# Performance work log

Measured on AMD Instinct MI355X. Metric: run time of the kernel, lower is better.

The kernel has to match this reference:

```python
import jax, jax.numpy as jnp
import numpy as np

H = 16  # GRU hidden size

def gru_dir(x, Wih, Whh, bih, bhh, reverse=False):
    # x: [B, T, D]; torch gate order: r, z, n
    def step(h, xt):
        gx = xt @ Wih.T + bih          # [B, 3H]
        gh = h @ Whh.T + bhh
        xr, xz, xn = jnp.split(gx, 3, axis=-1)
        hr, hz, hn = jnp.split(gh, 3, axis=-1)
        r = jax.nn.sigmoid(xr + hr)
        z = jax.nn.sigmoid(xz + hz)
        n = jnp.tanh(xn + r * hn)
        h_new = (1.0 - z) * n + z * h
        return h_new, h_new
    xs = jnp.swapaxes(x, 0, 1)         # [T, B, D]
    h0 = jnp.zeros((x.shape[0], H), x.dtype)
    _, hs = jax.lax.scan(step, h0, xs, reverse=reverse)
    return jnp.swapaxes(hs, 0, 1)      # [B, T, H]

def gru_bidir(x, pf, pb):
    f = gru_dir(x, *pf, reverse=False)
    b = gru_dir(x, *pb, reverse=True)
    return jnp.concatenate([f, b], axis=-1)   # [B, T, 2H]

def attention(h, Wa, ba, ctx):
    # h: [B, T, 2H]
    a = jnp.tanh(h @ Wa.T + ba)                # [B, T, 2H]
    w = jax.nn.softmax(a @ ctx, axis=1)        # [B, T]
    return jnp.einsum('bt,btd->bd', w, h), w

def setup_inputs() -> dict:
    key = jax.random.key(0)
    ks = iter(jax.random.split(key, 32))
    B, N, T, D, M = 64, 128, 128, 25, 16
    def p(shape, scale=0.1):
        return jax.random.normal(next(ks), shape, jnp.float32) * scale
    inp = {'x': jax.random.normal(next(ks), (B, N, T, D), jnp.float32)}
    # first bidirectional GRU (input 25)
    for sfx, din in [('1f', D), ('1b', D), ('2f', M), ('2b', M)]:
        inp['Wih' + sfx] = p((3 * H, din))
        inp['Whh' + sfx] = p((3 * H, H))
        inp['bih' + sfx] = p((3 * H,))
        inp['bhh' + sfx] = p((3 * H,))
    for sfx in ['1', '2']:
        inp['Wa' + sfx] = p((2 * H, 2 * H))
        inp['ba' + sfx] = p((2 * H,))
        inp['ctx' + sfx] = p((2 * H,))
    inp['Wm'] = p((M, 2 * H))
    inp['bm'] = p((M,))
    return inp

def reference(x, Wih1f, Whh1f, bih1f, bhh1f, Wih1b, Whh1b, bih1b, bhh1b,
              Wa1, ba1, ctx1, Wm, bm,
              Wih2f, Whh2f, bih2f, bhh2f, Wih2b, Whh2b, bih2b, bhh2b,
              Wa2, ba2, ctx2):
    B, N, T, D = x.shape
    xs = x.reshape(B * N, T, D)
    h1 = gru_bidir(xs, (Wih1f, Whh1f, bih1f, bhh1f), (Wih1b, Whh1b, bih1b, bhh1b))
    cv1, _ = attention(h1, Wa1, ba1, ctx1)          # [B*N, 2H]
    flow = (cv1 @ Wm.T + bm).reshape(B, N, -1)      # [B, N, M]
    h2 = gru_bidir(flow, (Wih2f, Whh2f, bih2f, bhh2f), (Wih2b, Whh2b, bih2b, bhh2b))
    cv2, _ = attention(h2, Wa2, ba2, ctx2)          # [B, 2H]
    return cv2
```

## Files before the change

### kernel.cpp

```cpp
#include <hip/hip_runtime.h>
#include <hip/hip_bf16.h>
#include <math.h>

#define TSTEPS 128
#define HD 16
#define AD 32
#define CHUNK 8
#define NCHK 16
#define H1W 36
#define SEQ_HALFS 4096
#define PH 264

#define SC1 1.44269504088896340736f
#define SC2 2.88539008177792681472f

typedef _Float16 h4 __attribute__((ext_vector_type(4)));
typedef _Float16 f16x8 __attribute__((ext_vector_type(8)));
typedef float f32x4 __attribute__((ext_vector_type(4)));

#if defined(__has_builtin)
#  if __has_builtin(__builtin_amdgcn_exp2f)
#    define EXP2F(x) __builtin_amdgcn_exp2f(x)
#  endif
#  if __has_builtin(__builtin_amdgcn_rcpf)
#    define RCPF(x) __builtin_amdgcn_rcpf(x)
#  endif
#  if __has_builtin(__builtin_amdgcn_global_load_lds)
#    define HAS_GLDS 1
#  endif
#endif
#ifndef EXP2F
#  define EXP2F(x) exp2f(x)
#endif
#ifndef RCPF
#  define RCPF(x) (1.0f / (x))
#endif

__device__ __forceinline__ float tanh_pre(float u) {
    return 1.0f - 2.0f * RCPF(EXP2F(u) + 1.0f);
}

#ifdef HAS_GLDS
typedef const __attribute__((address_space(1))) void gas_t;
typedef __attribute__((address_space(3))) void las_t;
#endif

template<int D>
__global__ __launch_bounds__(128, 1)
void gru_serial_kernel(
    const float* __restrict__ x,
    const float* __restrict__ Wih_f, const float* __restrict__ Whh_f,
    const float* __restrict__ bih_f, const float* __restrict__ bhh_f,
    const float* __restrict__ Wih_b, const float* __restrict__ Whh_b,
    const float* __restrict__ bih_b, const float* __restrict__ bhh_b,
    _Float16* __restrict__ ghist)
{
    constexpr int NSPAN = (8 * D) / 4;
    constexpr int TSPAN = 16 * NSPAN;
    constexpr int SPL   = (TSPAN + 63) / 64;

    __shared__ __align__(16) float    xraw[2][SPL * 64 * 4];
    __shared__ __align__(16) _Float16 xf16[2][2][16 * PH];

    const int tid  = threadIdx.x;
    const int lane = tid & 63;
    const int dir  = tid >> 6;
    const int dirw = __builtin_amdgcn_readfirstlane(dir);
    const int sd   = lane & 15;
    const int ug   = lane >> 4;

    const float* WihP = dir ? Wih_b : Wih_f;
    const float* WhhP = dir ? Whh_b : Whh_f;
    const float* bihP = dir ? bih_b : bih_f;
    const float* bhhP = dir ? bhh_b : bhh_f;

    h4 whhA[3];
    #pragma unroll
    for (int n = 0; n < 3; ++n) {
        const float sc = (n < 2) ? SC1 : SC2;
        const int g = 16 * n + sd;
        #pragma unroll
        for (int e = 0; e < 4; ++e)
            whhA[n][e] = (_Float16)(WhhP[g * HD + 4 * ug + e] * sc);
    }
    f16x8 wihA[3];
    #pragma unroll
    for (int n = 0; n < 3; ++n) {
        const float sc = (n < 2) ? SC1 : SC2;
        const int g = 16 * n + sd;
        const float bias = (n < 2) ? (bihP[g] + bhhP[g]) : bihP[g];
        #pragma unroll
        for (int e = 0; e < 8; ++e) {
            const int k = 8 * ug + e;
            wihA[n][e] = (k < D) ? (_Float16)(WihP[g * D + k] * sc)
                       : (k == D) ? (_Float16)(bias * sc)
                       : (_Float16)0.0f;
        }
    }
    float bhn[4];
    #pragma unroll
    for (int e = 0; e < 4; ++e)
        bhn[e] = bhhP[2 * HD + 4 * ug + e] * SC2;

    unsigned goff[SPL];
    #pragma unroll
    for (int j = 0; j < SPL; ++j) {
        int s = j * 64 + lane;
        if (s > TSPAN - 1) s = TSPAN - 1;
        const int sq2 = s / NSPAN;
        const int sp  = s - sq2 * NSPAN;
        goff[j] = (unsigned)(((blockIdx.x * 16 + sq2) * (TSTEPS * D) + sp * 4) * 4);
    }
    const char* xbytes = (const char*)x;

    const int sq  = lane >> 2;
    const int pst = lane & 3;

    h4 bcur = (h4){(_Float16)0.0f, (_Float16)0.0f, (_Float16)0.0f, (_Float16)0.0f};
    float hw[4] = {0.0f, 0.0f, 0.0f, 0.0f};
    _Float16* ghbase = ghist + (size_t)(blockIdx.x * 16 + sd) * SEQ_HALFS
                       + (size_t)(dir * 16 + 4 * ug) * 8;
    const f32x4 z4 = {0.f, 0.f, 0.f, 0.f};

    #define STAGE_RAW(cc)                                                     \
    {                                                                         \
        const unsigned toffB = (unsigned)((dir ? (TSTEPS - CHUNK - CHUNK*(cc)) \
                                               : (CHUNK*(cc))) * D * 4);      \
        _Pragma("unroll")                                                     \
        for (int j = 0; j < SPL; ++j) {                                       \
            const char* gp = xbytes + goff[j] + toffB;                        \
            char* lp = (char*)&xraw[dirw][0] + j * 1024;                      \
            STAGE_ONE(gp, lp);                                                \
        }                                                                     \
    }
    #ifdef HAS_GLDS
    #define STAGE_ONE(gp, lp) \
        __builtin_amdgcn_global_load_lds((gas_t*)(gp), (las_t*)(lp), 16, 0, 0);
    #else
    #define STAGE_ONE(gp, lp) \
        { const float4 v_ = *reinterpret_cast<const float4*>(gp); \
          *reinterpret_cast<float4*>((lp) + lane * 16) = v_; }
    #endif

    #define CONVERT(b)                                                        \
    {                                                                         \
        _Pragma("unroll")                                                     \
        for (int rr2 = 0; rr2 < 2; ++rr2) {                                   \
            const int row = 2 * pst + rr2;                                    \
            const float* rp = &xraw[dirw][0] + sq * (8 * D) + row * D;        \
            _Float16* wp = &xf16[dirw][b][sq * PH + row * 32];                \
            _Pragma("unroll")                                                 \
            for (int part = 0; part < 4; ++part) {                            \
                f16x8 w;                                                      \
                _Pragma("unroll")                                             \
                for (int e = 0; e < 8; ++e) {                                 \
                    const int k = part * 8 + e;                               \
                    w[e] = (k < D) ? (_Float16)rp[k]                          \
                         : (k == D) ? (_Float16)1.0f : (_Float16)0.0f;        \
                }                                                             \
                *reinterpret_cast<f16x8*>(wp + part * 8) = w;                 \
            }                                                                 \
        }                                                                     \
    }

    STAGE_RAW(0);
    asm volatile("s_waitcnt vmcnt(0)" ::: "memory");
    CONVERT(0);

    #pragma unroll 1
    for (int c = 0; c < NCHK; ++c) {
        if (c + 1 < NCHK) STAGE_RAW(c + 1);

        const _Float16* rdp = &xf16[dirw][c & 1][sd * PH + ug * 8];

        f16x8 hrow[4];
        f16x8 fA = *reinterpret_cast<const f16x8*>(rdp);
        #pragma unroll
        for (int ls = 0; ls < CHUNK; ++ls) {
            f16x8 fB;
            if (ls + 1 < CHUNK)
                fB = *reinterpret_cast<const f16x8*>(rdp + (ls + 1) * 32);

            const f32x4 gxr = __builtin_amdgcn_mfma_f32_16x16x32_f16(wihA[0], fA, z4, 0, 0, 0);
            const f32x4 gxz = __builtin_amdgcn_mfma_f32_16x16x32_f16(wihA[1], fA, z4, 0, 0, 0);
            const f32x4 gxn = __builtin_amdgcn_mfma_f32_16x16x32_f16(wihA[2], fA, z4, 0, 0, 0);
            const f32x4 ghr = __builtin_amdgcn_mfma_f32_16x16x16f16(whhA[0], bcur, z4, 0, 0, 0);
            const f32x4 ghz = __builtin_amdgcn_mfma_f32_16x16x16f16(whhA[1], bcur, z4, 0, 0, 0);
            const f32x4 ghn = __builtin_amdgcn_mfma_f32_16x16x16f16(whhA[2], bcur, z4, 0, 0, 0);

            #pragma unroll
            for (int e = 0; e < 4; ++e) {
                const float rr = RCPF(1.0f + EXP2F(-(gxr[e] + ghr[e])));
                const float zz = RCPF(1.0f + EXP2F(-(gxz[e] + ghz[e])));
                const float nv = tanh_pre(gxn[e] + rr * (ghn[e] + bhn[e]));
                hw[e] = nv + zz * (hw[e] - nv);
                const _Float16 hh16 = (_Float16)hw[e];
                bcur[e] = hh16;
                hrow[e][ls] = hh16;
            }
            if (ls + 1 < CHUNK) fA = fB;
        }

        const int cc2 = dir ? (NCHK - 1 - c) : c;
        _Float16* gp2 = ghbase + (size_t)cc2 * 256;
        #pragma unroll
        for (int e = 0; e < 4; ++e)
            *reinterpret_cast<f16x8*>(gp2 + e * 8) = hrow[e];

        if (c + 1 < NCHK) {
            asm volatile("s_waitcnt vmcnt(0)" ::: "memory");
            CONVERT((c + 1) & 1);
        }
    }
    #undef STAGE_RAW
    #undef STAGE_ONE
    #undef CONVERT
}

template<bool HAS_PROJ>
__global__ __launch_bounds__(128, 4)
void attn_kernel(
    const _Float16* __restrict__ ghist,
    const float* __restrict__ Wa, const float* __restrict__ ba,
    const float* __restrict__ ctxv,
    const float* __restrict__ Wm, const float* __restrict__ bm,
    float* __restrict__ out, int out_cols)
{
    __shared__ __align__(16) _Float16 h1[TSTEPS * H1W];
    __shared__ float w_sh[TSTEPS];
    __shared__ float red[4];
    __shared__ float cvp[4 * AD];

    const int tid  = threadIdx.x;
    const int lane = tid & 63;
    const int wave = tid >> 6;
    const int seq  = blockIdx.x;

    {
        const f16x8* src = reinterpret_cast<const f16x8*>(ghist + (size_t)seq * SEQ_HALFS);
        #pragma unroll
        for (int k = 0; k < 4; ++k) {
            const int idx = tid + k * 128;
            const f16x8 v = src[idx];
            const int u32 = idx & 31;
            const int tb  = (idx >> 5) * 8;
            const int flip = (u32 >= 16) ? 7 : 0;
            #pragma unroll
            for (int e = 0; e < 8; ++e)
                h1[(tb + (e ^ flip)) * H1W + u32] = v[e];
        }
    }
    __syncthreads();

    {
        const int t = tid;
        float hh[AD];
        const h4* hr = reinterpret_cast<const h4*>(&h1[t * H1W]);
        #pragma unroll
        for (int pp = 0; pp < AD / 4; ++pp) {
            const h4 v = hr[pp];
            #pragma unroll
            for (int e = 0; e < 4; ++e) hh[4 * pp + e] = (float)v[e];
        }
        float st = 0.0f;
        for (int i = 0; i < AD; ++i) {
            float a0 = ba[i], a1 = 0.f;
            const float* war = &Wa[i * AD];
            #pragma unroll
            for (int k = 0; k < AD; k += 2) {
                a0 += war[k] * hh[k];
                a1 += war[k + 1] * hh[k + 1];
            }
            st += tanh_pre(SC2 * (a0 + a1)) * ctxv[i];
        }
        float m = st;
        #pragma unroll
        for (int off = 32; off > 0; off >>= 1) m = fmaxf(m, __shfl_xor(m, off));
        if (lane == 0) red[wave] = m;
        __syncthreads();
        m = fmaxf(red[0], red[1]);
        const float e = EXP2F(SC1 * (st - m));
        float ssum = e;
        #pragma unroll
        for (int off = 32; off > 0; off >>= 1) ssum += __shfl_xor(ssum, off);
        if (lane == 0) red[2 + wave] = ssum;
        __syncthreads();
        const float Z = red[2] + red[3];
        w_sh[tid] = e * RCPF(Z);
    }
    __syncthreads();

    {
        const int g = tid >> 5, i = tid & 31;
        float acc = 0.0f;
        for (int k = 0; k < 32; ++k) {
            const int tt = g * 32 + k;
            acc += w_sh[tt] * (float)h1[tt * H1W + i];
        }
        cvp[g * AD + i] = acc;
    }
    __syncthreads();
    if (tid < AD)
        cvp[tid] = cvp[tid] + cvp[AD + tid] + cvp[2 * AD + tid] + cvp[3 * AD + tid];
    __syncthreads();

    if (HAS_PROJ) {
        if (tid < HD) {
            float acc = bm[tid];
            #pragma unroll
            for (int i = 0; i < AD; ++i) acc += Wm[tid * AD + i] * cvp[i];
            out[(size_t)seq * out_cols + tid] = acc;
        }
    } else {
        if (tid < AD) out[(size_t)seq * out_cols + tid] = cvp[tid];
    }
}

extern "C" void kernel_launch(void* const* d_in, const int* in_sizes, int n_in,
                              void* d_out, int out_size, void* d_ws, size_t ws_size,
                              hipStream_t stream) {
    const float* x     = (const float*)d_in[0];
    const float* Wih1f = (const float*)d_in[1];
    const float* Whh1f = (const float*)d_in[2];
    const float* bih1f = (const float*)d_in[3];
    const float* bhh1f = (const float*)d_in[4];
    const float* Wih1b = (const float*)d_in[5];
    const float* Whh1b = (const float*)d_in[6];
    const float* bih1b = (const float*)d_in[7];
    const float* bhh1b = (const float*)d_in[8];
    const float* Wih2f = (const float*)d_in[9];
    const float* Whh2f = (const float*)d_in[10];
    const float* bih2f = (const float*)d_in[11];
    const float* bhh2f = (const float*)d_in[12];
    const float* Wih2b = (const float*)d_in[13];
    const float* Whh2b = (const float*)d_in[14];
    const float* bih2b = (const float*)d_in[15];
    const float* bhh2b = (const float*)d_in[16];
    const float* Wa1   = (const float*)d_in[17];
    const float* ba1   = (const float*)d_in[18];
    const float* ctx1  = (const float*)d_in[19];
    const float* Wa2   = (const float*)d_in[20];
    const float* ba2   = (const float*)d_in[21];
    const float* ctx2  = (const float*)d_in[22];
    const float* Wm    = (const float*)d_in[23];
    const float* bm    = (const float*)d_in[24];

    float* flow = (float*)d_ws;
    const size_t histOff = 1u << 20;
    _Float16* ghist = (_Float16*)((char*)d_ws + histOff);
    float* outp = (float*)d_out;

    gru_serial_kernel<25><<<512, 128, 0, stream>>>(
        x, Wih1f, Whh1f, bih1f, bhh1f, Wih1b, Whh1b, bih1b, bhh1b, ghist);
    attn_kernel<true><<<8192, 128, 0, stream>>>(
        ghist, Wa1, ba1, ctx1, Wm, bm, flow, 16);

    gru_serial_kernel<16><<<4, 128, 0, stream>>>(
        flow, Wih2f, Whh2f, bih2f, bhh2f, Wih2b, Whh2b, bih2b, bhh2b, ghist);
    attn_kernel<false><<<64, 128, 0, stream>>>(
        ghist, Wa2, ba2, ctx2, nullptr, nullptr, outp, 32);
}
```

Before: 184.7 us.

## Use register-staged input prefetch for second GRU and relax vmcnt wait

Adds a second GRU kernel variant for the small D=16 pass that loads the next chunk's inputs into registers with plain global loads, then converts them into the double-buffered LDS stage after the chunk's recurrence. This replaces the global-to-LDS staging path for that launch. The first GRU keeps the old path but waits for fewer outstanding loads (vmcnt(4) instead of vmcnt(0)) before converting, and adds a compiler barrier after issuing the prefetch. The partial wait risks reading unfinished staged data if the count does not match the loads the conversion depends on.

```diff
diff --git a/kernel.cpp b/kernel.cpp
--- a/kernel.cpp
+++ b/kernel.cpp
@@ -46,8 +46,23 @@
 #endif
 
 template<int D>
+__device__ __forceinline__ void store_row(_Float16* wp, const float* v) {
+    #pragma unroll
+    for (int part = 0; part < 4; ++part) {
+        f16x8 w;
+        #pragma unroll
+        for (int e = 0; e < 8; ++e) {
+            const int k = part * 8 + e;
+            w[e] = (k < D) ? (_Float16)v[k]
+                 : (k == D) ? (_Float16)1.0f : (_Float16)0.0f;
+        }
+        *reinterpret_cast<f16x8*>(wp + part * 8) = w;
+    }
+}
+
+template<int D>
 __global__ __launch_bounds__(128, 1)
-void gru_serial_kernel(
+void gru_serial_glds(
     const float* __restrict__ x,
     const float* __restrict__ Wih_f, const float* __restrict__ Whh_f,
     const float* __restrict__ bih_f, const float* __restrict__ bhh_f,
@@ -170,6 +185,7 @@
     #pragma unroll 1
     for (int c = 0; c < NCHK; ++c) {
         if (c + 1 < NCHK) STAGE_RAW(c + 1);
+        asm volatile("" ::: "memory");
 
         const _Float16* rdp = &xf16[dirw][c & 1][sd * PH + ug * 8];
 
@@ -208,13 +224,144 @@
             *reinterpret_cast<f16x8*>(gp2 + e * 8) = hrow[e];
 
         if (c + 1 < NCHK) {
-            asm volatile("s_waitcnt vmcnt(0)" ::: "memory");
+            asm volatile("s_waitcnt vmcnt(4)" ::: "memory");
             CONVERT((c + 1) & 1);
         }
     }
     #undef STAGE_RAW
     #undef STAGE_ONE
     #undef CONVERT
+}
+
+template<int D>
+__global__ __launch_bounds__(128, 1)
+void gru_serial_scalar(
+    const float* __restrict__ x,
+    const float* __restrict__ Wih_f, const float* __restrict__ Whh_f,
+    const float* __restrict__ bih_f, const float* __restrict__ bhh_f,
+    const float* __restrict__ Wih_b, const float* __restrict__ Whh_b,
+    const float* __restrict__ bih_b, const float* __restrict__ bhh_b,
+    _Float16* __restrict__ ghist)
+{
+    __shared__ __align__(16) _Float16 xstage[2 * 2 * 16 * PH];
+
+    const int tid  = threadIdx.x;
+    const int lane = tid & 63;
+    const int dir  = tid >> 6;
+    const int sd   = lane & 15;
+    const int ug   = lane >> 4;
+
+    const float* WihP = dir ? Wih_b : Wih_f;
+    const float* WhhP = dir ? Whh_b : Whh_f;
+    const float* bihP = dir ? bih_b : bih_f;
+    const float* bhhP = dir ? bhh_b : bhh_f;
+
+    h4 whhA[3];
+    #pragma unroll
+    for (int n = 0; n < 3; ++n) {
+        const float sc = (n < 2) ? SC1 : SC2;
+        const int g = 16 * n + sd;
+        #pragma unroll
+        for (int e = 0; e < 4; ++e)
+            whhA[n][e] = (_Float16)(WhhP[g * HD + 4 * ug + e] * sc);
+    }
+    f16x8 wihA[3];
+    #pragma unroll
+    for (int n = 0; n < 3; ++n) {
+        const float sc = (n < 2) ? SC1 : SC2;
+        const int g = 16 * n + sd;
+        const float bias = (n < 2) ? (bihP[g] + bhhP[g]) : bihP[g];
+        #pragma unroll
+        for (int e = 0; e < 8; ++e) {
+            const int k = 8 * ug + e;
+            wihA[n][e] = (k < D) ? (_Float16)(WihP[g * D + k] * sc)
+                       : (k == D) ? (_Float16)(bias * sc)
+                       : (_Float16)0.0f;
+        }
+    }
+    float bhn[4];
+    #pragma unroll
+    for (int e = 0; e < 4; ++e)
+        bhn[e] = bhhP[2 * HD + 4 * ug + e] * SC2;
+
+    const int sst = lane >> 2;
+    const int pst = lane & 3;
+    const int ls0 = 2 * pst, ls1 = ls0 + 1;
+    const float* xseq = x + (size_t)(blockIdx.x * 16 + sst) * (TSTEPS * D);
+
+    _Float16* mybuf = xstage + dir * (2 * 16 * PH);
+    _Float16* wpr0  = mybuf + sst * PH + ls0 * 32;
+    _Float16* wpr1  = mybuf + sst * PH + ls1 * 32;
+
+    {
+        const int t0 = dir ? (TSTEPS - 1 - ls0) : ls0;
+        const int t1 = dir ? (TSTEPS - 1 - ls1) : ls1;
+        const float* r0 = xseq + (size_t)t0 * D;
+        const float* r1 = xseq + (size_t)t1 * D;
+        float rA[D], rB[D];
+        #pragma unroll
+        for (int k = 0; k < D; ++k) { rA[k] = r0[k]; rB[k] = r1[k]; }
+        store_row<D>(wpr0, rA);
+        store_row<D>(wpr1, rB);
+    }
+
+    h4 bcur = (h4){(_Float16)0.0f, (_Float16)0.0f, (_Float16)0.0f, (_Float16)0.0f};
+    float hw[4] = {0.0f, 0.0f, 0.0f, 0.0f};
+    _Float16* ghbase = ghist + (size_t)(blockIdx.x * 16 + sd) * SEQ_HALFS
+                       + (size_t)(dir * 16 + 4 * ug) * 8;
+    const f32x4 z4 = {0.f, 0.f, 0.f, 0.f};
+
+    #pragma unroll 1
+    for (int c = 0; c < NCHK; ++c) {
+        float rA[D], rB[D];
+        if (c + 1 < NCHK) {
+            const int s0 = (c + 1) * CHUNK + ls0;
+            const int s1 = (c + 1) * CHUNK + ls1;
+            const int t0 = dir ? (TSTEPS - 1 - s0) : s0;
+            const int t1 = dir ? (TSTEPS - 1 - s1) : s1;
+            const float* r0 = xseq + (size_t)t0 * D;
+            const float* r1 = xseq + (size_t)t1 * D;
+            #pragma unroll
+            for (int k = 0; k < D; ++k) { rA[k] = r0[k]; rB[k] = r1[k]; }
+        }
+
+        const _Float16* rdp = mybuf + (c & 1) * (16 * PH) + sd * PH + ug * 8;
+        f16x8 hrow[4];
+        #pragma unroll
+        for (int ls = 0; ls < CHUNK; ++ls) {
+            const f16x8 frag = *reinterpret_cast<const f16x8*>(rdp + ls * 32);
+
+            const f32x4 gxr = __builtin_amdgcn_mfma_f32_16x16x32_f16(wihA[0], frag, z4, 0, 0, 0);
+            const f32x4 gxz = __builtin_amdgcn_mfma_f32_16x16x32_f16(wihA[1], frag, z4, 0, 0, 0);
+            const f32x4 gxn = __builtin_amdgcn_mfma_f32_16x16x32_f16(wihA[2], frag, z4, 0, 0, 0);
+            const f32x4 ghr = __builtin_amdgcn_mfma_f32_16x16x16f16(whhA[0], bcur, z4, 0, 0, 0);
+            const f32x4 ghz = __builtin_amdgcn_mfma_f32_16x16x16f16(whhA[1], bcur, z4, 0, 0, 0);
+            const f32x4 ghn = __builtin_amdgcn_mfma_f32_16x16x16f16(whhA[2], bcur, z4, 0, 0, 0);
+
+            #pragma unroll
+            for (int e = 0; e < 4; ++e) {
+                const float rr = RCPF(1.0f + EXP2F(-(gxr[e] + ghr[e])));
+                const float zz = RCPF(1.0f + EXP2F(-(gxz[e] + ghz[e])));
+                const float nv = tanh_pre(gxn[e] + rr * (ghn[e] + bhn[e]));
+                hw[e] = nv + zz * (hw[e] - nv);
+                const _Float16 hh16 = (_Float16)hw[e];
+                bcur[e] = hh16;
+                hrow[e][ls] = hh16;
+            }
+        }
+
+        const int cc = dir ? (NCHK - 1 - c) : c;
+        _Float16* gp = ghbase + (size_t)cc * 256;
+        #pragma unroll
+        for (int e = 0; e < 4; ++e)
+            *reinterpret_cast<f16x8*>(gp + e * 8) = hrow[e];
+
+        if (c + 1 < NCHK) {
+            const int bs = ((c + 1) & 1) * (16 * PH);
+            store_row<D>(wpr0 + bs, rA);
+            store_row<D>(wpr1 + bs, rB);
+        }
+    }
 }
 
 template<bool HAS_PROJ>
@@ -350,12 +497,12 @@
     _Float16* ghist = (_Float16*)((char*)d_ws + histOff);
     float* outp = (float*)d_out;
 
-    gru_serial_kernel<25><<<512, 128, 0, stream>>>(
+    gru_serial_glds<25><<<512, 128, 0, stream>>>(
         x, Wih1f, Whh1f, bih1f, bhh1f, Wih1b, Whh1b, bih1b, bhh1b, ghist);
     attn_kernel<true><<<8192, 128, 0, stream>>>(
         ghist, Wa1, ba1, ctx1, Wm, bm, flow, 16);
 
-    gru_serial_kernel<16><<<4, 128, 0, stream>>>(
+    gru_serial_scalar<16><<<4, 128, 0, stream>>>(
         flow, Wih2f, Whh2f, bih2f, bhh2f, Wih2b, Whh2b, bih2b, bhh2b, ghist);
     attn_kernel<false><<<64, 128, 0, stream>>>(
         ghist, Wa2, ba2, ctx2, nullptr, nullptr, outp, 32);
```

Result: faster. 154.0 us (-16.6%).
